# Kernel optimization log

Hardware: AMD Instinct MI355X
Metric: run time of the kernel (lower is better)

## Reference

```python
import jax, jax.numpy as jnp
import numpy as np
import math

D_MODEL = 1024
N_HEADS = 16
SEQ = 2048
BATCH = 2


def setup_inputs() -> dict:
    key = jax.random.key(0)
    ks = jax.random.split(key, 7)
    scale = 1.0 / math.sqrt(D_MODEL)
    return {
        "q": jax.random.normal(ks[0], (SEQ, BATCH, D_MODEL), jnp.float32),
        "k": jax.random.normal(ks[1], (SEQ, BATCH, D_MODEL), jnp.float32),
        "v": jax.random.normal(ks[2], (SEQ, BATCH, D_MODEL), jnp.float32),
        "in_proj_w": jax.random.normal(ks[3], (3 * D_MODEL, D_MODEL), jnp.float32) * scale,
        "in_proj_b": jax.random.normal(ks[4], (3 * D_MODEL,), jnp.float32) * 0.01,
        "out_proj_w": jax.random.normal(ks[5], (D_MODEL, D_MODEL), jnp.float32) * scale,
        "out_proj_b": jax.random.normal(ks[6], (D_MODEL,), jnp.float32) * 0.01,
    }


def reference(q, k, v, in_proj_w, in_proj_b, out_proj_w, out_proj_b):
    # q, k, v: (S, B, D) seq-first layout as in the torch module
    S, B, D = q.shape
    H = N_HEADS
    dk = D // H
    wq, wk, wv = jnp.split(in_proj_w, 3, axis=0)   # each (D, D)
    bq, bk, bv = jnp.split(in_proj_b, 3, axis=0)   # each (D,)
    qp = q @ wq.T + bq
    kp = k @ wk.T + bk
    vp = v @ wv.T + bv
    # (S, B, D) -> (S, B*H, dk) -> (B*H, S, dk)
    def to_heads(x, s):
        return x.reshape(s, B * H, dk).transpose(1, 0, 2)
    qh = to_heads(qp, S)
    kh = to_heads(kp, k.shape[0])
    vh = to_heads(vp, v.shape[0])
    # scores: (B*H, Sq, Sk)
    scores = jnp.einsum('bqd,bkd->bqk', qh, kh) / math.sqrt(dk)
    probs = jax.nn.softmax(scores, axis=-1)
    attn = jnp.einsum('bqk,bkd->bqd', probs, vh)   # (B*H, S, dk)
    # (B*H, S, dk) -> (S, B*H, dk) -> (S*B, D)
    attn = attn.transpose(1, 0, 2).reshape(S * B, D)
    out = attn @ out_proj_w.T + out_proj_b
    return out.reshape(S, B, D)
```

## Files before the change

### kernel.cpp

```cpp
#include <hip/hip_runtime.h>
#include <math.h>

#define SEQ    2048
#define BATCH  2
#define DMODEL 1024
#define NHEADS 16
#define DK     64

typedef __attribute__((ext_vector_type(8))) short  bf16x8;
typedef __attribute__((ext_vector_type(4))) float  f32x4;
typedef __attribute__((ext_vector_type(8))) unsigned short u16x8;

#define GLD16(gp, lp) __builtin_amdgcn_global_load_lds(                      \
    (__attribute__((address_space(1))) void*)(gp),                            \
    (__attribute__((address_space(3))) void*)(lp), 16, 0, 0)

__device__ inline unsigned short f2bf(float f) {
    unsigned int u = __float_as_uint(f);
    u += 0x7fffu + ((u >> 16) & 1u);
    return (unsigned short)(u >> 16);
}

__device__ inline unsigned int pk2bf(float a, float b) {
#if __has_builtin(__builtin_amdgcn_cvt_pk_bf16_f32)
    typedef __attribute__((ext_vector_type(2))) __bf16 v2bf;
    v2bf r = __builtin_amdgcn_cvt_pk_bf16_f32(a, b);
    unsigned int u; __builtin_memcpy(&u, &r, 4); return u;
#else
    return (unsigned int)f2bf(a) | ((unsigned int)f2bf(b) << 16);
#endif
}

__device__ inline float fast_exp2(float x) {
#if __has_builtin(__builtin_amdgcn_exp2f)
    return __builtin_amdgcn_exp2f(x);
#else
    return __expf(x * 0.69314718055994531f);
#endif
}

#define WS_QB   0u
#define WS_KB   4194304u
#define WS_VB   8388608u
#define WS_WIB  12582912u
#define WS_WOB  15728640u
#define WS_QH   16777216u
#define WS_KH   20971520u
#define WS_VT   25165824u
#define WS_ATT  29360128u

__global__ __launch_bounds__(256) void cast_all_kernel(
    const float* __restrict__ q, const float* __restrict__ k,
    const float* __restrict__ v, const float* __restrict__ w_in,
    const float* __restrict__ w_out, unsigned short* __restrict__ ws)
{
    const int gid = blockIdx.x * 256 + threadIdx.x;
    const float* src; unsigned short* dst;
    if (gid < 524288)       { int g = gid;           src = q     + (size_t)g*8; dst = ws + WS_QB  + (size_t)g*8; }
    else if (gid < 1048576) { int g = gid - 524288;  src = k     + (size_t)g*8; dst = ws + WS_KB  + (size_t)g*8; }
    else if (gid < 1572864) { int g = gid - 1048576; src = v     + (size_t)g*8; dst = ws + WS_VB  + (size_t)g*8; }
    else if (gid < 1966080) { int g = gid - 1572864; src = w_in  + (size_t)g*8; dst = ws + WS_WIB + (size_t)g*8; }
    else                    { int g = gid - 1966080; src = w_out + (size_t)g*8; dst = ws + WS_WOB + (size_t)g*8; }
    float4 a = *(const float4*)src;
    float4 b = *(const float4*)(src + 4);
    u16x8 o;
    o[0]=f2bf(a.x); o[1]=f2bf(a.y); o[2]=f2bf(a.z); o[3]=f2bf(a.w);
    o[4]=f2bf(b.x); o[5]=f2bf(b.y); o[6]=f2bf(b.z); o[7]=f2bf(b.w);
    *(u16x8*)dst = o;
}

__global__ __launch_bounds__(256) void qkv_gemm_kernel(
    const unsigned short* __restrict__ ws_in, const float* __restrict__ bias,
    unsigned short* __restrict__ ws_out)
{
    __shared__ unsigned short As[128*32];
    __shared__ unsigned short Bs[128*32];

    const int t    = threadIdx.x;
    const int lane = t & 63;
    const int w    = t >> 6;
    const int lrow = lane & 15;
    const int quad = lane >> 4;
    const int wm   = (w >> 1) * 64;
    const int wn   = (w & 1) * 64;

    const int n0    = blockIdx.x * 128;
    const int m0    = blockIdx.y * 128;
    const int which = n0 >> 10;

    const unsigned short* A = ws_in + WS_QB + (size_t)which * 4194304u;
    const unsigned short* B = ws_in + WS_WIB;

    const int srow = t >> 2;
    const int scc  = (t & 3) ^ ((t >> 3) & 3);
    const unsigned short* gA0 = A + (size_t)(m0 + srow) * 1024 + scc * 8;
    const unsigned short* gA1 = A + (size_t)(m0 + 64 + srow) * 1024 + scc * 8;
    const unsigned short* gB0 = B + (size_t)(n0 + srow) * 1024 + scc * 8;
    const unsigned short* gB1 = B + (size_t)(n0 + 64 + srow) * 1024 + scc * 8;

    f32x4 acc[4][4] = {};

    #pragma unroll 1
    for (int kt = 0; kt < 1024; kt += 32) {
        __syncthreads();
        GLD16(gA0, As + (size_t)t * 8);
        GLD16(gA1, As + (size_t)(t + 256) * 8);
        GLD16(gB0, Bs + (size_t)t * 8);
        GLD16(gB1, Bs + (size_t)(t + 256) * 8);
        gA0 += 32; gA1 += 32; gB0 += 32; gB1 += 32;
        __syncthreads();

        bf16x8 af[4], bf[4];
        #pragma unroll
        for (int mt = 0; mt < 4; ++mt) {
            const int r = wm + mt*16 + lrow;
            af[mt] = *(const bf16x8*)(As + r*32 + ((quad ^ ((r>>1)&3))*8));
        }
        #pragma unroll
        for (int nt = 0; nt < 4; ++nt) {
            const int r = wn + nt*16 + lrow;
            bf[nt] = *(const bf16x8*)(Bs + r*32 + ((quad ^ ((r>>1)&3))*8));
        }
        #pragma unroll
        for (int mt = 0; mt < 4; ++mt)
            #pragma unroll
            for (int nt = 0; nt < 4; ++nt)
                acc[mt][nt] = __builtin_amdgcn_mfma_f32_16x16x32_bf16(
                    af[mt], bf[nt], acc[mt][nt], 0, 0, 0);
    }

    unsigned short* dstQK = ws_out + WS_QH + (size_t)which * 4194304u;
    unsigned short* dstV  = ws_out + WS_VT;
    const float qscale = 0.18033688011112042f;

    #pragma unroll
    for (int nt = 0; nt < 4; ++nt) {
        const int n = n0 + wn + nt*16 + lrow;
        const float bn = bias[n];
        const int h = (n & 1023) >> 6;
        const int d = n & 63;
        #pragma unroll
        for (int mt = 0; mt < 4; ++mt) {
            if (which < 2) {
                #pragma unroll
                for (int r = 0; r < 4; ++r) {
                    const int m = m0 + wm + mt*16 + quad*4 + r;
                    const int s = m >> 1, b = m & 1;
                    float val = acc[mt][nt][r] + bn;
                    if (which == 0) val *= qscale;
                    dstQK[((size_t)((b<<4) + h) * 2048 + s) * 64 + d] = f2bf(val);
                }
            } else {
                const int m_base = m0 + wm + mt*16 + quad*4;
                const int s0 = m_base >> 1;
                unsigned int pk0 = pk2bf(acc[mt][nt][0] + bn, acc[mt][nt][2] + bn);
                unsigned int pk1 = pk2bf(acc[mt][nt][1] + bn, acc[mt][nt][3] + bn);
                *(unsigned int*)(dstV + ((size_t)h*64 + d)*2048 + s0)        = pk0;
                *(unsigned int*)(dstV + ((size_t)(16 + h)*64 + d)*2048 + s0) = pk1;
            }
        }
    }
}

__global__ __launch_bounds__(256) void attn_mfma_kernel(
    const unsigned short* __restrict__ qh, const unsigned short* __restrict__ kh,
    const unsigned short* __restrict__ vt, unsigned short* __restrict__ attn)
{
    __shared__ unsigned short Qs[64*64];
    __shared__ unsigned short Ks[64*64];
    __shared__ unsigned short Vts[64*64];
    __shared__ unsigned short Ps[64*64];

    const int t    = threadIdx.x;
    const int lane = t & 63;
    const int w    = t >> 6;
    const int lrow = lane & 15;
    const int quad = lane >> 4;

    const int qt = blockIdx.x;
    const int bh = blockIdx.y;

    const unsigned short* Qg = qh + ((size_t)bh * 2048 + qt * 64) * 64;
    const unsigned short* Kb = kh + (size_t)bh * 2048 * 64;
    const unsigned short* Vb = vt + (size_t)bh * 64 * 2048;

    #pragma unroll
    for (int i = 0; i < 2; ++i) {
        const int c = i*256 + t;
        const int row = c >> 3, cc = (c & 7) ^ (row & 7);
        GLD16(Qg + (size_t)row*64 + cc*8, Qs + (size_t)c*8);
    }

    f32x4 O[4] = {};
    float m_i = -INFINITY, l_i = 0.f;

    #pragma unroll 1
    for (int ktile = 0; ktile < 32; ++ktile) {
        __syncthreads();
        const unsigned short* Kg = Kb + (size_t)ktile * 64 * 64;
        const unsigned short* Vg = Vb + (size_t)ktile * 64;
        #pragma unroll
        for (int i = 0; i < 2; ++i) {
            const int c = i*256 + t;
            const int row = c >> 3, cc = (c & 7) ^ (row & 7);
            GLD16(Kg + (size_t)row*64   + cc*8, Ks  + (size_t)c*8);
            GLD16(Vg + (size_t)row*2048 + cc*8, Vts + (size_t)c*8);
        }
        __syncthreads();

        f32x4 ST[4] = {};
        #pragma unroll
        for (int kk = 0; kk < 2; ++kk) {
            bf16x8 kf[4], qf;
            #pragma unroll
            for (int m = 0; m < 4; ++m) {
                const int r = m*16 + lrow;
                kf[m] = *(const bf16x8*)(Ks + r*64 + (((kk*4+quad) ^ (r&7))*8));
            }
            {
                const int r = w*16 + lrow;
                qf = *(const bf16x8*)(Qs + r*64 + (((kk*4+quad) ^ (r&7))*8));
            }
            #pragma unroll
            for (int m = 0; m < 4; ++m)
                ST[m] = __builtin_amdgcn_mfma_f32_16x16x32_bf16(
                    kf[m], qf, ST[m], 0, 0, 0);
        }

        float mx;
        {
            float mm;
            #pragma unroll
            for (int m = 0; m < 4; ++m) {
                float m01 = fmaxf(fmaxf(ST[m][0], ST[m][1]),
                                  fmaxf(ST[m][2], ST[m][3]));
                mm = (m == 0) ? m01 : fmaxf(mm, m01);
            }
            mm = fmaxf(mm, __shfl_xor(mm, 16, 64));
            mm = fmaxf(mm, __shfl_xor(mm, 32, 64));
            mx = mm;
        }

        float al;
        if (__any(mx > m_i)) {
            const float mn = fmaxf(m_i, mx);
            al = fast_exp2(m_i - mn);
            m_i = mn;
            #pragma unroll
            for (int dt = 0; dt < 4; ++dt)
                O[dt] *= al;
        } else {
            al = 1.f;
        }

        {
            const int prow = w*16 + lrow;
            const float mn = m_i;
            float rsum = 0.f;
            #pragma unroll
            for (int m = 0; m < 4; ++m) {
                const float p0 = fast_exp2(ST[m][0] - mn);
                const float p1 = fast_exp2(ST[m][1] - mn);
                const float p2 = fast_exp2(ST[m][2] - mn);
                const float p3 = fast_exp2(ST[m][3] - mn);
                rsum += (p0 + p1) + (p2 + p3);
                uint2 pk;
                pk.x = pk2bf(p0, p1);
                pk.y = pk2bf(p2, p3);
                const int sc = (m*2 + (quad >> 1)) ^ (prow & 7);
                *(uint2*)(Ps + prow*64 + sc*8 + (quad & 1)*4) = pk;
            }
            rsum += __shfl_xor(rsum, 16, 64);
            rsum += __shfl_xor(rsum, 32, 64);
            l_i = l_i*al + rsum;
        }

        #pragma unroll
        for (int kk = 0; kk < 2; ++kk) {
            bf16x8 vf[4], pf;
            #pragma unroll
            for (int dt = 0; dt < 4; ++dt) {
                const int r = dt*16 + lrow;
                vf[dt] = *(const bf16x8*)(Vts + r*64 + (((kk*4+quad) ^ (r&7))*8));
            }
            {
                const int r = w*16 + lrow;
                pf = *(const bf16x8*)(Ps + r*64 + (((kk*4+quad) ^ (r&7))*8));
            }
            #pragma unroll
            for (int dt = 0; dt < 4; ++dt)
                O[dt] = __builtin_amdgcn_mfma_f32_16x16x32_bf16(
                    vf[dt], pf, O[dt], 0, 0, 0);
        }
    }

    const int b_ = bh >> 4, h_ = bh & 15;
    const float inv = 1.f / l_i;
    const int s_ = qt*64 + w*16 + lrow;
    unsigned short* dst = attn + ((size_t)(s_*2 + b_)) * 1024 + h_*64;
    #pragma unroll
    for (int dt = 0; dt < 4; ++dt) {
        uint2 pk;
        pk.x = pk2bf(O[dt][0]*inv, O[dt][1]*inv);
        pk.y = pk2bf(O[dt][2]*inv, O[dt][3]*inv);
        *(uint2*)(dst + dt*16 + quad*4) = pk;
    }
}

__global__ __launch_bounds__(256) void out_gemm_kernel(
    const unsigned short* __restrict__ A, const unsigned short* __restrict__ B,
    const float* __restrict__ bias, float* __restrict__ out)
{
    __shared__ unsigned short As[64*32];
    __shared__ unsigned short Bs[128*32];

    const int t    = threadIdx.x;
    const int lane = t & 63;
    const int w    = t >> 6;
    const int lrow = lane & 15;
    const int quad = lane >> 4;
    const int wn   = (w >> 1) * 64;
    const int wm   = (w & 1) * 32;

    const int n0 = blockIdx.x * 128;
    const int m0 = blockIdx.y * 64;

    const int srow = t >> 2;
    const int scc  = (t & 3) ^ ((t >> 3) & 3);
    const unsigned short* gA0 = A + (size_t)(m0 + srow) * 1024 + scc * 8;
    const unsigned short* gB0 = B + (size_t)(n0 + srow) * 1024 + scc * 8;
    const unsigned short* gB1 = B + (size_t)(n0 + 64 + srow) * 1024 + scc * 8;

    f32x4 acc[2][4] = {};

    #pragma unroll 1
    for (int kt = 0; kt < 1024; kt += 32) {
        __syncthreads();
        GLD16(gA0, As + (size_t)t * 8);
        GLD16(gB0, Bs + (size_t)t * 8);
        GLD16(gB1, Bs + (size_t)(t + 256) * 8);
        gA0 += 32; gB0 += 32; gB1 += 32;
        __syncthreads();

        bf16x8 af[2], bf[4];
        #pragma unroll
        for (int mt = 0; mt < 2; ++mt) {
            const int r = wm + mt*16 + lrow;
            af[mt] = *(const bf16x8*)(As + r*32 + ((quad ^ ((r>>1)&3))*8));
        }
        #pragma unroll
        for (int nt = 0; nt < 4; ++nt) {
            const int r = wn + nt*16 + lrow;
            bf[nt] = *(const bf16x8*)(Bs + r*32 + ((quad ^ ((r>>1)&3))*8));
        }
        #pragma unroll
        for (int mt = 0; mt < 2; ++mt)
            #pragma unroll
            for (int nt = 0; nt < 4; ++nt)
                acc[mt][nt] = __builtin_amdgcn_mfma_f32_16x16x32_bf16(
                    af[mt], bf[nt], acc[mt][nt], 0, 0, 0);
    }

    #pragma unroll
    for (int nt = 0; nt < 4; ++nt) {
        const int n = n0 + wn + nt*16 + lrow;
        const float bn = bias[n];
        #pragma unroll
        for (int mt = 0; mt < 2; ++mt) {
            #pragma unroll
            for (int r = 0; r < 4; ++r) {
                const int m = m0 + wm + mt*16 + quad*4 + r;
                out[(size_t)m * 1024 + n] = acc[mt][nt][r] + bn;
            }
        }
    }
}

extern "C" void kernel_launch(void* const* d_in, const int* in_sizes, int n_in,
                              void* d_out, int out_size, void* d_ws, size_t ws_size,
                              hipStream_t stream) {
    const float* q     = (const float*)d_in[0];
    const float* k     = (const float*)d_in[1];
    const float* v     = (const float*)d_in[2];
    const float* w_in  = (const float*)d_in[3];
    const float* b_in  = (const float*)d_in[4];
    const float* w_out = (const float*)d_in[5];
    const float* b_out = (const float*)d_in[6];
    float* out = (float*)d_out;

    unsigned short* ws = (unsigned short*)d_ws;

    cast_all_kernel<<<8192, 256, 0, stream>>>(q, k, v, w_in, w_out, ws);
    qkv_gemm_kernel<<<dim3(24, 32), 256, 0, stream>>>(ws, b_in, ws);
    attn_mfma_kernel<<<dim3(32, 32), 256, 0, stream>>>(
        ws + WS_QH, ws + WS_KH, ws + WS_VT, ws + WS_ATT);
    out_gemm_kernel<<<dim3(8, 64), 256, 0, stream>>>(
        ws + WS_ATT, ws + WS_WOB, b_out, out);
}
```

Baseline: 247.9 us.

## Double-buffer K/V tiles in attention with register-resident Q and lazy rescale

The attention kernel now keeps two LDS buffers for K and V. It issues the global-to-LDS load of the next tile before computing on the current one, so there is one barrier per iteration instead of two and the load latency is meant to overlap the MFMA and softmax work. Q fragments are loaded into registers once instead of being re-read from LDS every tile. MFMA sections are wrapped in s_setprio, and the online-softmax rescale is skipped unless the new max exceeds the running max by more than 8 in log2 units. The cost is twice the K/V LDS footprint, which may lower occupancy, and the rescale threshold lets unnormalized exponentials grow up to 2^8 before the accumulator is rescaled.

```diff
diff --git a/kernel.cpp b/kernel.cpp
--- a/kernel.cpp
+++ b/kernel.cpp
@@ -167,8 +167,8 @@
     const unsigned short* __restrict__ vt, unsigned short* __restrict__ attn)
 {
     __shared__ unsigned short Qs[64*64];
-    __shared__ unsigned short Ks[64*64];
-    __shared__ unsigned short Vts[64*64];
+    __shared__ unsigned short Ks[2][64*64];
+    __shared__ unsigned short Vts[2][64*64];
     __shared__ unsigned short Ps[64*64];
 
     const int t    = threadIdx.x;
@@ -188,43 +188,56 @@
     for (int i = 0; i < 2; ++i) {
         const int c = i*256 + t;
         const int row = c >> 3, cc = (c & 7) ^ (row & 7);
-        GLD16(Qg + (size_t)row*64 + cc*8, Qs + (size_t)c*8);
+        GLD16(Qg + (size_t)row*64   + cc*8, Qs + (size_t)c*8);
+        GLD16(Kb + (size_t)row*64   + cc*8, &Ks[0][0]  + (size_t)c*8);
+        GLD16(Vb + (size_t)row*2048 + cc*8, &Vts[0][0] + (size_t)c*8);
+    }
+    __syncthreads();
+
+    bf16x8 qf[2];
+    #pragma unroll
+    for (int kk = 0; kk < 2; ++kk) {
+        const int r = w*16 + lrow;
+        qf[kk] = *(const bf16x8*)(Qs + r*64 + (((kk*4+quad) ^ (r&7))*8));
     }
 
     f32x4 O[4] = {};
     float m_i = -INFINITY, l_i = 0.f;
 
+    int buf = 0;
     #pragma unroll 1
     for (int ktile = 0; ktile < 32; ++ktile) {
-        __syncthreads();
-        const unsigned short* Kg = Kb + (size_t)ktile * 64 * 64;
-        const unsigned short* Vg = Vb + (size_t)ktile * 64;
-        #pragma unroll
-        for (int i = 0; i < 2; ++i) {
-            const int c = i*256 + t;
-            const int row = c >> 3, cc = (c & 7) ^ (row & 7);
-            GLD16(Kg + (size_t)row*64   + cc*8, Ks  + (size_t)c*8);
-            GLD16(Vg + (size_t)row*2048 + cc*8, Vts + (size_t)c*8);
-        }
-        __syncthreads();
+        if (ktile < 31) {
+            const unsigned short* Kg = Kb + (size_t)(ktile + 1) * 64 * 64;
+            const unsigned short* Vg = Vb + (size_t)(ktile + 1) * 64;
+            unsigned short* Kn = &Ks[buf ^ 1][0];
+            unsigned short* Vn = &Vts[buf ^ 1][0];
+            #pragma unroll
+            for (int i = 0; i < 2; ++i) {
+                const int c = i*256 + t;
+                const int row = c >> 3, cc = (c & 7) ^ (row & 7);
+                GLD16(Kg + (size_t)row*64   + cc*8, Kn + (size_t)c*8);
+                GLD16(Vg + (size_t)row*2048 + cc*8, Vn + (size_t)c*8);
+            }
+        }
+        const unsigned short* Kc = &Ks[buf][0];
+        const unsigned short* Vc = &Vts[buf][0];
 
         f32x4 ST[4] = {};
         #pragma unroll
         for (int kk = 0; kk < 2; ++kk) {
-            bf16x8 kf[4], qf;
+            bf16x8 kf[4];
             #pragma unroll
             for (int m = 0; m < 4; ++m) {
                 const int r = m*16 + lrow;
-                kf[m] = *(const bf16x8*)(Ks + r*64 + (((kk*4+quad) ^ (r&7))*8));
-            }
-            {
-                const int r = w*16 + lrow;
-                qf = *(const bf16x8*)(Qs + r*64 + (((kk*4+quad) ^ (r&7))*8));
-            }
+                kf[m] = *(const bf16x8*)(Kc + r*64 + (((kk*4+quad) ^ (r&7))*8));
+            }
+            __builtin_amdgcn_s_setprio(1);
             #pragma unroll
             for (int m = 0; m < 4; ++m)
                 ST[m] = __builtin_amdgcn_mfma_f32_16x16x32_bf16(
-                    kf[m], qf, ST[m], 0, 0, 0);
+                    kf[m], qf[kk], ST[m], 0, 0, 0);
+            __builtin_amdgcn_s_setprio(0);
         }
 
         float mx;
@@ -241,16 +254,14 @@
             mx = mm;
         }
 
-        float al;
-        if (__any(mx > m_i)) {
+        float al = 1.f;
+        if (__any(mx > m_i + 8.f)) {
             const float mn = fmaxf(m_i, mx);
             al = fast_exp2(m_i - mn);
             m_i = mn;
             #pragma unroll
             for (int dt = 0; dt < 4; ++dt)
                 O[dt] *= al;
-        } else {
-            al = 1.f;
         }
 
         {
@@ -281,17 +292,22 @@
             #pragma unroll
             for (int dt = 0; dt < 4; ++dt) {
                 const int r = dt*16 + lrow;
-                vf[dt] = *(const bf16x8*)(Vts + r*64 + (((kk*4+quad) ^ (r&7))*8));
+                vf[dt] = *(const bf16x8*)(Vc + r*64 + (((kk*4+quad) ^ (r&7))*8));
             }
             {
                 const int r = w*16 + lrow;
                 pf = *(const bf16x8*)(Ps + r*64 + (((kk*4+quad) ^ (r&7))*8));
             }
+            __builtin_amdgcn_s_setprio(1);
             #pragma unroll
             for (int dt = 0; dt < 4; ++dt)
                 O[dt] = __builtin_amdgcn_mfma_f32_16x16x32_bf16(
                     vf[dt], pf, O[dt], 0, 0, 0);
-        }
+            __builtin_amdgcn_s_setprio(0);
+        }
+
+        __syncthreads();
+        buf ^= 1;
     }
 
     const int b_ = bh >> 4, h_ = bh & 15;
```

Result: slower. 265.2 us (+7.0%).
